# Kernel tuning notes

Measured on AMD Instinct MI355X. Metric: run time of the kernel, lower is better.

Reference implementation:

```python
import jax, jax.numpy as jnp
import numpy as np

N, L, D1, D2, K, C, T = 50000, 1024, 512, 256, 64, 2, 49


def setup_inputs() -> dict:
    key = jax.random.key(0)
    ks = jax.random.split(key, 20)
    s = 0.02
    return {
        "h": jax.random.normal(ks[0], (N, L), dtype=jnp.float32),
        "tabular": jax.random.normal(ks[1], (1, T), dtype=jnp.float32),
        "label": 1,
        # fc: Linear(1024,512)+ReLU
        "W_fc": jax.random.normal(ks[2], (L, D1)) * s, "b_fc": jnp.zeros((D1,)),
        # gated attention net
        "Wa": jax.random.normal(ks[3], (D1, D2)) * s, "ba": jnp.zeros((D2,)),
        "Wb": jax.random.normal(ks[4], (D1, D2)) * s, "bb": jnp.zeros((D2,)),
        "Wc": jax.random.normal(ks[5], (D2, 1)) * s, "bc": jnp.zeros((1,)),
        # per-class instance classifiers Linear(512,2), stacked [C, D1, 2]
        "W_inst": jax.random.normal(ks[6], (C, D1, 2)) * s, "b_inst": jnp.zeros((C, 2)),
        # MultiHeadAttention (1 head)
        "W_img": jax.random.normal(ks[7], (D1, 1)) * s, "b_img": jnp.zeros((1,)),
        "W_tab": jax.random.normal(ks[8], (T, T)) * s, "b_tab": jnp.zeros((T,)),
        # bag classifier Linear(512+49, 2)
        "W_cls": jax.random.normal(ks[9], (D1 + T, C)) * s, "b_cls": jnp.zeros((C,)),
    }


def _forward(h, tabular, label, W_fc, b_fc, Wa, ba, Wb, bb, Wc, bc,
             W_inst, b_inst, W_img, b_img, W_tab, b_tab, W_cls, b_cls):
    # attention_net: fc + ReLU then gated attention
    h512 = jax.nn.relu(h @ W_fc + b_fc)                       # [N, 512]
    a = jnp.tanh(h512 @ Wa + ba)                              # [N, 256]
    b = jax.nn.sigmoid(h512 @ Wb + bb)                        # [N, 256]
    A = ((a * b) @ Wc + bc).T                                 # [1, N]
    A_raw = A
    A = jax.nn.softmax(A, axis=1)                             # [1, N]

    # instance eval: top-k positive / top-k negative selection + tiny classifier + CE
    scores = A[0]                                             # [N]
    _, top_p_ids = jax.lax.top_k(scores, K)
    _, top_n_ids = jax.lax.top_k(-scores, K)
    all_inst = jnp.concatenate([h512[top_p_ids], h512[top_n_ids]], axis=0)  # [2K, 512]
    targets = jnp.concatenate([jnp.ones((K,), jnp.int32), jnp.zeros((K,), jnp.int32)])

    def inst_loss(Wi, bi):
        logits = all_inst @ Wi + bi                           # [2K, 2]
        logp = jax.nn.log_softmax(logits, axis=1)
        return -jnp.mean(logp[jnp.arange(2 * K), targets])

    losses = jax.vmap(inst_loss)(W_inst, b_inst)              # [C]
    onehot = jax.nn.one_hot(label, C, dtype=losses.dtype)
    total_inst_loss = jnp.sum(onehot * losses)                # only in-class classifier contributes

    # attention pooling
    M = A @ h512                                              # [1, 512]

    # MultiHeadAttention (1 head): gated image feature + softmax-gated tabular feature
    img_score = jax.nn.sigmoid(M @ W_img + b_img)             # [1, 1]
    tab_score = jax.nn.softmax(tabular @ W_tab + b_tab, axis=1)  # [1, 49]
    concat = jnp.concatenate([img_score * M, tab_score * tabular], axis=1)  # [1, 561]

    logits = concat @ W_cls + b_cls                           # [1, 2]
    Y_prob = jax.nn.softmax(logits, axis=1)
    Y_hat = jnp.argmax(logits, axis=1)
    return logits, Y_prob, Y_hat, A_raw, total_inst_loss


def reference(h, tabular, label, W_fc, b_fc, Wa, ba, Wb, bb, Wc, bc,
              W_inst, b_inst, W_img, b_img, W_tab, b_tab, W_cls, b_cls):
    return _forward(h, tabular, label, W_fc, b_fc, Wa, ba, Wb, bb, Wc, bc,
                    W_inst, b_inst, W_img, b_img, W_tab, b_tab, W_cls, b_cls)
```

## Files before the change

kernel.cpp:

```cpp
#include <hip/hip_runtime.h>
#include <stdint.h>

typedef __bf16 bf16x8 __attribute__((ext_vector_type(8)));
typedef float f32x4 __attribute__((ext_vector_type(4)));
typedef unsigned short u16;
typedef unsigned int u32;

#define N_INST 50000
#define NPAD   50048
#define LIN    1024
#define D1     512
#define D2     256
#define TOPK   64
#define TDIM   49
#define NBIN   65536
#define CAND_MAX 8192
#define ZERO_DW (520 + 128 + 16 + NBIN)

__device__ __forceinline__ float b2f(u16 u) {
    union { float f; u32 i; } x; x.i = ((u32)u) << 16; return x.f;
}
__device__ __forceinline__ u16 f2b(float f) {
    union { float f; u32 i; } x; x.f = f;
    u32 r = x.i + 0x7FFFu + ((x.i >> 16) & 1u);
    return (u16)(r >> 16);
}
__device__ __forceinline__ void gload16(const void* g, void* l) {
    __builtin_amdgcn_global_load_lds((const __attribute__((address_space(1))) void*)g,
                                     (__attribute__((address_space(3))) void*)l, 16, 0, 0);
}
__device__ __forceinline__ u32 swz(int row, int bytecol) {
    return (u32)(row * 128 + (bytecol ^ ((row & 7) << 4)));
}

__global__ void pack_w(const float* __restrict__ W_fc, const float* __restrict__ Wa,
                       const float* __restrict__ Wb, u16* __restrict__ WfcT,
                       u16* __restrict__ WaT, u16* __restrict__ WbT, u32* __restrict__ zbase) {
    int gt = blockIdx.x * blockDim.x + threadIdx.x;
    int nthr = gridDim.x * blockDim.x;
    for (int z = gt; z < ZERO_DW; z += nthr) zbase[z] = 0u;
    for (int e = gt; e < D1 * LIN; e += nthr) {
        int n = e >> 10, k = e & 1023;
        WfcT[e] = f2b(W_fc[(size_t)k * D1 + n]);
    }
    for (int f = gt; f < D2 * D1; f += nthr) {
        int j = f >> 9, k = f & 511;
        WaT[f] = f2b(Wa[(size_t)k * D2 + j]);
        WbT[f] = f2b(Wb[(size_t)k * D2 + j]);
    }
}

__global__ __launch_bounds__(512, 2)
void gemm_fc(const float* __restrict__ h, const u16* __restrict__ WfcT,
             const float* __restrict__ b_fc, u16* __restrict__ h512) {
    __shared__ __align__(16) u16 lA[128 * 64];
    __shared__ __align__(16) u16 lB[256 * 64];
    const int tid = threadIdx.x;
    const int lane = tid & 63, wid = tid >> 6;
    const int wr = wid >> 2, wc = wid & 3;
    const int lanelo = lane & 15, lanehi = lane >> 4;
    const int row0 = blockIdx.y * 128;
    const int col0 = blockIdx.x * 256;

    const int arow = tid >> 2;
    const int aseg = tid & 3;
    int srow = row0 + arow; if (srow >= N_INST) srow = N_INST - 1;
    const float* abase = h + (size_t)srow * LIN + aseg * 16;
    u16* aw0 = (u16*)((char*)lA + swz(arow, aseg * 32));
    u16* aw1 = (u16*)((char*)lA + swz(arow, aseg * 32 + 16));

    f32x4 acc[4][4];
    const f32x4 z4 = {0.f, 0.f, 0.f, 0.f};
    #pragma unroll
    for (int m = 0; m < 4; ++m)
        #pragma unroll
        for (int n = 0; n < 4; ++n) acc[m][n] = z4;

    float4 a0, a1, a2, a3;
    { const float4* ap = (const float4*)abase; a0 = ap[0]; a1 = ap[1]; a2 = ap[2]; a3 = ap[3]; }

    for (int kt = 0; kt < LIN / 64; ++kt) {
        #pragma unroll
        for (int q = 0; q < 4; ++q) {
            int c = tid + 512 * q;
            int col = c >> 3, d8 = c & 7;
            int k8 = d8 ^ (col & 7);
            gload16(WfcT + (size_t)(col0 + col) * LIN + kt * 64 + k8 * 8, (char*)lB + c * 16);
        }
        {
            bf16x8 w0, w1;
            w0[0] = (__bf16)a0.x; w0[1] = (__bf16)a0.y; w0[2] = (__bf16)a0.z; w0[3] = (__bf16)a0.w;
            w0[4] = (__bf16)a1.x; w0[5] = (__bf16)a1.y; w0[6] = (__bf16)a1.z; w0[7] = (__bf16)a1.w;
            w1[0] = (__bf16)a2.x; w1[1] = (__bf16)a2.y; w1[2] = (__bf16)a2.z; w1[3] = (__bf16)a2.w;
            w1[4] = (__bf16)a3.x; w1[5] = (__bf16)a3.y; w1[6] = (__bf16)a3.z; w1[7] = (__bf16)a3.w;
            *(bf16x8*)aw0 = w0;
            *(bf16x8*)aw1 = w1;
        }
        __syncthreads();
        if (kt + 1 < LIN / 64) {
            const float4* ap = (const float4*)(abase + (kt + 1) * 64);
            a0 = ap[0]; a1 = ap[1]; a2 = ap[2]; a3 = ap[3];
        }
        #pragma unroll
        for (int kk = 0; kk < 2; ++kk) {
            bf16x8 af[4], bfr[4];
            #pragma unroll
            for (int m = 0; m < 4; ++m) {
                int row = wr * 64 + m * 16 + lanelo;
                af[m] = *(const bf16x8*)((char*)lA + swz(row, kk * 64 + lanehi * 16));
            }
            #pragma unroll
            for (int n = 0; n < 4; ++n) {
                int col = wc * 64 + n * 16 + lanelo;
                bfr[n] = *(const bf16x8*)((char*)lB + swz(col, kk * 64 + lanehi * 16));
            }
            #pragma unroll
            for (int m = 0; m < 4; ++m)
                #pragma unroll
                for (int n = 0; n < 4; ++n)
                    acc[m][n] = __builtin_amdgcn_mfma_f32_16x16x32_bf16(af[m], bfr[n], acc[m][n], 0, 0, 0);
        }
        __syncthreads();
    }
    #pragma unroll
    for (int n = 0; n < 4; ++n) {
        int col = col0 + wc * 64 + n * 16 + lanelo;
        float bias = b_fc[col];
        #pragma unroll
        for (int m = 0; m < 4; ++m) {
            int rbase = row0 + wr * 64 + m * 16 + 4 * lanehi;
            #pragma unroll
            for (int r = 0; r < 4; ++r) {
                float v = acc[m][n][r] + bias;
                v = v > 0.f ? v : 0.f;
                h512[(size_t)(rbase + r) * D1 + col] = f2b(v);
            }
        }
    }
}

__global__ __launch_bounds__(512, 2)
void gemm_attn(const u16* __restrict__ h512, const u16* __restrict__ WaT,
               const u16* __restrict__ WbT, const float* __restrict__ ba,
               const float* __restrict__ bb, const float* __restrict__ Wc,
               const float* __restrict__ bc, float* __restrict__ araw,
               u32* __restrict__ uarr, u32* __restrict__ hist,
               float* __restrict__ Zacc, float* __restrict__ Mpart) {
    __shared__ __align__(16) u16 lA[128 * 64];
    __shared__ __align__(16) u16 lBa[256 * 64];
    __shared__ __align__(16) u16 lBb[256 * 64];
    __shared__ float rsum[128];
    __shared__ float sW[128];
    const int tid = threadIdx.x;
    const int lane = tid & 63, wid = tid >> 6;
    const int wr = wid >> 2, wc4 = wid & 3;
    const int lanelo = lane & 15, lanehi = lane >> 4;
    const int row0 = blockIdx.x * 128;

    f32x4 accA[4][4], accB[4][4];
    const f32x4 z4 = {0.f, 0.f, 0.f, 0.f};
    for (int m = 0; m < 4; ++m)
        for (int n = 0; n < 4; ++n) { accA[m][n] = z4; accB[m][n] = z4; }

    for (int kt = 0; kt < D1 / 64; ++kt) {
        #pragma unroll
        for (int q = 0; q < 2; ++q) {
            int c = tid + 512 * q;
            int row = c >> 3, d8 = c & 7;
            int k8 = d8 ^ (row & 7);
            gload16(h512 + (size_t)(row0 + row) * D1 + kt * 64 + k8 * 8, (char*)lA + c * 16);
        }
        #pragma unroll
        for (int q = 0; q < 4; ++q) {
            int c = tid + 512 * q;
            int col = c >> 3, d8 = c & 7;
            int k8 = d8 ^ (col & 7);
            gload16(WaT + (size_t)col * D1 + kt * 64 + k8 * 8, (char*)lBa + c * 16);
            gload16(WbT + (size_t)col * D1 + kt * 64 + k8 * 8, (char*)lBb + c * 16);
        }
        __syncthreads();
        #pragma unroll
        for (int kk = 0; kk < 2; ++kk) {
            bf16x8 af[4], ga[4], gb[4];
            #pragma unroll
            for (int m = 0; m < 4; ++m) {
                int row = wr * 64 + m * 16 + lanelo;
                af[m] = *(const bf16x8*)((char*)lA + swz(row, kk * 64 + lanehi * 16));
            }
            #pragma unroll
            for (int n = 0; n < 4; ++n) {
                int col = wc4 * 64 + n * 16 + lanelo;
                u32 off = swz(col, kk * 64 + lanehi * 16);
                ga[n] = *(const bf16x8*)((char*)lBa + off);
                gb[n] = *(const bf16x8*)((char*)lBb + off);
            }
            #pragma unroll
            for (int m = 0; m < 4; ++m)
                #pragma unroll
                for (int n = 0; n < 4; ++n) {
                    accA[m][n] = __builtin_amdgcn_mfma_f32_16x16x32_bf16(af[m], ga[n], accA[m][n], 0, 0, 0);
                    accB[m][n] = __builtin_amdgcn_mfma_f32_16x16x32_bf16(af[m], gb[n], accB[m][n], 0, 0, 0);
                }
        }
        __syncthreads();
    }

    if (tid < 128) rsum[tid] = 0.f;
    __syncthreads();

    float baR[4], bbR[4], wcR[4];
    #pragma unroll
    for (int n = 0; n < 4; ++n) {
        int j = wc4 * 64 + n * 16 + lanelo;
        baR[n] = ba[j]; bbR[n] = bb[j]; wcR[n] = Wc[j];
    }
    #pragma unroll
    for (int m = 0; m < 4; ++m) {
        #pragma unroll
        for (int r = 0; r < 4; ++r) {
            float s = 0.f;
            #pragma unroll
            for (int n = 0; n < 4; ++n) {
                float av = accA[m][n][r] + baR[n];
                float bv = accB[m][n][r] + bbR[n];
                float p = tanhf(av) / (1.f + expf(-bv));
                s += p * wcR[n];
            }
            s += __shfl_xor(s, 1); s += __shfl_xor(s, 2);
            s += __shfl_xor(s, 4); s += __shfl_xor(s, 8);
            if (lanelo == 0) atomicAdd(&rsum[wr * 64 + m * 16 + 4 * lanehi + r], s);
        }
    }
    __syncthreads();

    if (tid < 128) {
        int rg = row0 + tid;
        float e = 0.f;
        if (rg < N_INST) {
            float a = rsum[tid] + bc[0];
            araw[rg] = a;
            u32 bits = __float_as_uint(a);
            u32 key = (bits & 0x80000000u) ? ~bits : (bits | 0x80000000u);
            uarr[rg] = key;
            atomicAdd(&hist[key >> 16], 1u);
            e = expf(a);
        }
        sW[tid] = e;
    }
    __syncthreads();
    if (tid < 128) {
        float e = sW[tid];
        for (int o = 32; o > 0; o >>= 1) e += __shfl_xor(e, o);
        if (lane == 0) atomicAdd(Zacc, e);
    }
    float accM = 0.f;
    for (int i = 0; i < 128; ++i)
        accM += sW[i] * b2f(h512[(size_t)(row0 + i) * D1 + tid]);
    atomicAdd(&Mpart[tid], accM);
}

__global__ void topk_collect(const u32* __restrict__ hist, const u32* __restrict__ uarr,
                             int* __restrict__ ctl, int* __restrict__ ids,
                             u32* __restrict__ cV0, int* __restrict__ cI0,
                             u32* __restrict__ cV1, int* __restrict__ cI1) {
    __shared__ int part[256];
    __shared__ int sp0, sb0, sp1, sb1;
    const int t = threadIdx.x;
    const uint4* h4 = (const uint4*)hist;
    int s = 0;
    for (int j = 0; j < 64; ++j) {
        uint4 v = h4[t * 64 + j];
        s += (int)(v.x + v.y + v.z + v.w);
    }
    part[t] = s;
    __syncthreads();
    for (int off = 1; off < 256; off <<= 1) {
        int v = part[t];
        int a = (t >= off) ? part[t - off] : 0;
        __syncthreads();
        part[t] = v + a;
        __syncthreads();
    }
    int run = part[t] - s;
    for (int j = 0; j < 64; ++j) {
        uint4 v = h4[t * 64 + j];
        int c4[4]; c4[0] = (int)v.x; c4[1] = (int)v.y; c4[2] = (int)v.z; c4[3] = (int)v.w;
        #pragma unroll
        for (int e = 0; e < 4; ++e) {
            int cnt = c4[e];
            if (cnt > 0) {
                int b = t * 256 + j * 4 + e;
                int less = run, greater = N_INST - run - cnt;
                if (greater < TOPK && greater + cnt >= TOPK) { sp0 = b; sb0 = greater; }
                if (less < TOPK && less + cnt >= TOPK)       { sp1 = b; sb1 = less; }
            }
            run += cnt;
        }
    }
    __syncthreads();
    const int p0 = sp0, p1 = sp1;
    if (blockIdx.x == 0 && t == 0) { ctl[0] = sp0; ctl[1] = sb0; ctl[2] = sp1; ctl[3] = sb1; }

    int gt = blockIdx.x * blockDim.x + t;
    int nthr = gridDim.x * blockDim.x;
    for (int i = gt; i < N_INST; i += nthr) {
        u32 v = uarr[i];
        int b = (int)(v >> 16);
        if (b > p0)       { int p = atomicAdd(&ctl[8], 1);  ids[p] = i; }
        else if (b == p0) { int p = atomicAdd(&ctl[9], 1);  if (p < CAND_MAX) { cV0[p] = v; cI0[p] = i; } }
        if (b < p1)       { int p = atomicAdd(&ctl[10], 1); ids[TOPK + p] = i; }
        else if (b == p1) { int p = atomicAdd(&ctl[11], 1); if (p < CAND_MAX) { cV1[p] = v; cI1[p] = i; } }
    }
}

__global__ void tail_fused(const int* __restrict__ ctl,
                           const u32* __restrict__ cV0, const int* __restrict__ cI0,
                           const u32* __restrict__ cV1, const int* __restrict__ cI1,
                           int* __restrict__ ids, const u16* __restrict__ h512,
                           const float* __restrict__ W_inst, const float* __restrict__ b_inst,
                           const int* __restrict__ label, const float* __restrict__ Mpart,
                           const float* __restrict__ Zacc, const float* __restrict__ tabular,
                           const float* __restrict__ W_img, const float* __restrict__ b_img,
                           const float* __restrict__ W_tab, const float* __restrict__ b_tab,
                           const float* __restrict__ W_cls, const float* __restrict__ b_cls,
                           float* __restrict__ d_out) {
    __shared__ int h8[256];
    __shared__ int eq[2048];
    __shared__ int s_d1, s_k1, s_d2, s_fill, s_eqc;
    __shared__ float lsum;
    __shared__ float sM[512];
    __shared__ float stab[TDIM];
    __shared__ float red0[256], red1[256];
    __shared__ float simg;
    const int tid = threadIdx.x;
    const int lane = tid & 63, wid = tid >> 6;

    for (int mode = 0; mode < 2; ++mode) {
        int basem = ctl[mode * 2 + 1];
        int need = TOPK - basem;
        int ccnt = ctl[9 + mode * 2];
        if (ccnt > CAND_MAX) ccnt = CAND_MAX;
        const u32* cV = mode ? cV1 : cV0;
        const int* cI = mode ? cI1 : cI0;
        int* dst = ids + mode * TOPK;
        h8[tid] = 0; __syncthreads();
        for (int i = tid; i < ccnt; i += 256) atomicAdd(&h8[(cV[i] >> 8) & 255u], 1);
        __syncthreads();
        if (tid == 0) {
            int acc = 0, d, k = need;
            if (mode == 0) { for (d = 255; d >= 0; --d) { acc += h8[d]; if (acc >= k) break; } }
            else           { for (d = 0; d < 256; ++d)  { acc += h8[d]; if (acc >= k) break; } }
            s_d1 = d; s_k1 = k - (acc - h8[d]);
        }
        __syncthreads();
        int d1 = s_d1, k1 = s_k1;
        h8[tid] = 0; __syncthreads();
        for (int i = tid; i < ccnt; i += 256) {
            u32 v = cV[i];
            if (((v >> 8) & 255u) == (u32)d1) atomicAdd(&h8[v & 255u], 1);
        }
        __syncthreads();
        if (tid == 0) {
            int acc = 0, d, k = k1;
            if (mode == 0) { for (d = 255; d >= 0; --d) { acc += h8[d]; if (acc >= k) break; } }
            else           { for (d = 0; d < 256; ++d)  { acc += h8[d]; if (acc >= k) break; } }
            s_d2 = d; s_fill = 0; s_eqc = 0;
        }
        __syncthreads();
        u32 vth = ((u32)ctl[mode * 2] << 16) | ((u32)d1 << 8) | (u32)s_d2;
        for (int i = tid; i < ccnt; i += 256) {
            u32 v = cV[i];
            bool better = mode == 0 ? (v > vth) : (v < vth);
            if (better)        { int p = atomicAdd(&s_fill, 1); dst[basem + p] = cI[i]; }
            else if (v == vth) { int p = atomicAdd(&s_eqc, 1);  if (p < 2048) eq[p] = cI[i]; }
        }
        __syncthreads();
        if (tid == 0) {
            int have = basem + s_fill;
            int rem = TOPK - have;
            int m = s_eqc < 2048 ? s_eqc : 2048;
            int last = -1;
            for (int q = 0; q < rem; ++q) {
                int best = 0x7FFFFFFF;
                for (int s = 0; s < m; ++s) { int ix = eq[s]; if (ix > last && ix < best) best = ix; }
                dst[have + q] = best; last = best;
            }
        }
        __syncthreads();
    }

    if (tid == 0) lsum = 0.f;
    __syncthreads();
    const int lab = label[0];
    const float* W = W_inst + (size_t)lab * (D1 * 2);
    const float b0 = b_inst[lab * 2 + 0], b1 = b_inst[lab * 2 + 1];
    for (int i = 0; i < 32; ++i) {
        int r = wid * 32 + i;
        int row = ids[r];
        float s0 = 0.f, s1 = 0.f;
        for (int s = 0; s < 8; ++s) {
            int j = lane + 64 * s;
            float hv = b2f(h512[(size_t)row * D1 + j]);
            s0 += hv * W[j * 2 + 0];
            s1 += hv * W[j * 2 + 1];
        }
        for (int o = 32; o > 0; o >>= 1) { s0 += __shfl_xor(s0, o); s1 += __shfl_xor(s1, o); }
        if (lane == 0) {
            float l0 = s0 + b0, l1 = s1 + b1;
            float mx = fmaxf(l0, l1);
            float lse = mx + logf(expf(l0 - mx) + expf(l1 - mx));
            float lt = (r < TOPK) ? l1 : l0;
            atomicAdd(&lsum, lse - lt);
        }
    }
    __syncthreads();
    if (tid == 0) d_out[50005] = lsum / 128.f;

    float invZ = 1.f / Zacc[0];
    sM[tid] = Mpart[tid] * invZ;
    sM[tid + 256] = Mpart[tid + 256] * invZ;
    red0[tid] = sM[tid] * W_img[tid] + sM[tid + 256] * W_img[tid + 256];
    __syncthreads();
    for (int o = 128; o > 0; o >>= 1) { if (tid < o) red0[tid] += red0[tid + o]; __syncthreads(); }
    if (tid == 0) simg = 1.f / (1.f + expf(-(red0[0] + b_img[0])));
    if (tid < TDIM) {
        float t = b_tab[tid];
        for (int kx = 0; kx < TDIM; ++kx) t += tabular[kx] * W_tab[kx * TDIM + tid];
        stab[tid] = t;
    }
    __syncthreads();
    if (tid == 0) {
        float mx = stab[0];
        for (int o = 1; o < TDIM; ++o) mx = fmaxf(mx, stab[o]);
        float ss = 0.f;
        for (int o = 0; o < TDIM; ++o) { float e = expf(stab[o] - mx); stab[o] = e; ss += e; }
        for (int o = 0; o < TDIM; ++o) stab[o] = (stab[o] / ss) * tabular[o];
    }
    __syncthreads();
    float img = simg;
    float a0 = 0.f, a1 = 0.f;
    for (int j = tid; j < D1 + TDIM; j += 256) {
        float w = (j < D1) ? img * sM[j] : stab[j - D1];
        a0 += w * W_cls[j * 2 + 0];
        a1 += w * W_cls[j * 2 + 1];
    }
    red0[tid] = a0; red1[tid] = a1;
    __syncthreads();
    for (int o = 128; o > 0; o >>= 1) {
        if (tid < o) { red0[tid] += red0[tid + o]; red1[tid] += red1[tid + o]; }
        __syncthreads();
    }
    if (tid == 0) {
        float l0 = red0[0] + b_cls[0];
        float l1 = red1[0] + b_cls[1];
        d_out[0] = l0; d_out[1] = l1;
        float mx = fmaxf(l0, l1);
        float e0 = expf(l0 - mx), e1 = expf(l1 - mx);
        d_out[2] = e0 / (e0 + e1);
        d_out[3] = e1 / (e0 + e1);
        d_out[4] = (l1 > l0) ? 1.f : 0.f;
    }
}

extern "C" void kernel_launch(void* const* d_in, const int* in_sizes, int n_in,
                              void* d_out, int out_size, void* d_ws, size_t ws_size,
                              hipStream_t stream) {
    const float* h       = (const float*)d_in[0];
    const float* tabular = (const float*)d_in[1];
    const int*   label   = (const int*)d_in[2];
    const float* W_fc    = (const float*)d_in[3];
    const float* b_fc    = (const float*)d_in[4];
    const float* Wa      = (const float*)d_in[5];
    const float* ba      = (const float*)d_in[6];
    const float* Wb      = (const float*)d_in[7];
    const float* bb      = (const float*)d_in[8];
    const float* Wc      = (const float*)d_in[9];
    const float* bc      = (const float*)d_in[10];
    const float* W_inst  = (const float*)d_in[11];
    const float* b_inst  = (const float*)d_in[12];
    const float* W_img   = (const float*)d_in[13];
    const float* b_img   = (const float*)d_in[14];
    const float* W_tab   = (const float*)d_in[15];
    const float* b_tab   = (const float*)d_in[16];
    const float* W_cls   = (const float*)d_in[17];
    const float* b_cls   = (const float*)d_in[18];
    float* out = (float*)d_out;

    u16* h512 = (u16*)d_ws;
    u16* WfcT = h512 + (size_t)NPAD * D1;
    u16* WaT  = WfcT + (size_t)D1 * LIN;
    u16* WbT  = WaT + (size_t)D2 * D1;
    u32* uarr = (u32*)(WbT + (size_t)D2 * D1);
    float* accum = (float*)(uarr + NPAD);
    float* Zacc  = accum;
    float* Mpart = accum + 8;
    int* ids = (int*)(accum + 8 + D1);
    int* ctl = ids + 128;
    u32* hist = (u32*)(ctl + 16);
    u32* cV0 = hist + NBIN;
    int* cI0 = (int*)(cV0 + CAND_MAX);
    u32* cV1 = (u32*)(cI0 + CAND_MAX);
    int* cI1 = (int*)(cV1 + CAND_MAX);

    pack_w<<<dim3(256), dim3(256), 0, stream>>>(W_fc, Wa, Wb, WfcT, WaT, WbT, (u32*)accum);
    gemm_fc<<<dim3(2, NPAD / 128), dim3(512), 0, stream>>>(h, WfcT, b_fc, h512);
    gemm_attn<<<dim3(NPAD / 128), dim3(512), 0, stream>>>(
        h512, WaT, WbT, ba, bb, Wc, bc, out + 5, uarr, hist, Zacc, Mpart);
    topk_collect<<<dim3(128), dim3(256), 0, stream>>>(hist, uarr, ctl, ids, cV0, cI0, cV1, cI1);
    tail_fused<<<dim3(1), dim3(256), 0, stream>>>(
        ctl, cV0, cI0, cV1, cI1, ids, h512, W_inst, b_inst, label,
        Mpart, Zacc, tabular, W_img, b_img, W_tab, b_tab, W_cls, b_cls, out);
}
```

Baseline: 308.7 us.

## Load fc A operand straight to registers and double-buffer B tiles in LDS

The fc GEMM no longer stages the fp32 activations through LDS. Each wave loads its A rows directly from global memory in the MFMA fragment layout, converts them to bf16 in registers and prefetches the next k-tile. The weight tile B is double-buffered in shared memory, so each iteration needs one barrier instead of two. The trade-off is that the four waves sharing a row group each fetch the same A rows, which multiplies global/L2 traffic for the largest input. The larger prefetch register set also risks spills or lower occupancy.

```diff
diff --git a/kernel.cpp b/kernel.cpp
--- a/kernel.cpp
+++ b/kernel.cpp
@@ -53,8 +53,7 @@
 __global__ __launch_bounds__(512, 2)
 void gemm_fc(const float* __restrict__ h, const u16* __restrict__ WfcT,
              const float* __restrict__ b_fc, u16* __restrict__ h512) {
-    __shared__ __align__(16) u16 lA[128 * 64];
-    __shared__ __align__(16) u16 lB[256 * 64];
+    __shared__ __align__(16) u16 lB[2][256 * 64];
     const int tid = threadIdx.x;
     const int lane = tid & 63, wid = tid >> 6;
     const int wr = wid >> 2, wc = wid & 3;
@@ -62,12 +61,20 @@
     const int row0 = blockIdx.y * 128;
     const int col0 = blockIdx.x * 256;
 
-    const int arow = tid >> 2;
-    const int aseg = tid & 3;
-    int srow = row0 + arow; if (srow >= N_INST) srow = N_INST - 1;
-    const float* abase = h + (size_t)srow * LIN + aseg * 16;
-    u16* aw0 = (u16*)((char*)lA + swz(arow, aseg * 32));
-    u16* aw1 = (u16*)((char*)lA + swz(arow, aseg * 32 + 16));
+    const float* arow0;
+    const float* arow1;
+    const float* arow2;
+    const float* arow3;
+    {
+        int r0 = row0 + wr * 64 + 0 * 16 + lanelo; if (r0 >= N_INST) r0 = N_INST - 1;
+        int r1 = row0 + wr * 64 + 1 * 16 + lanelo; if (r1 >= N_INST) r1 = N_INST - 1;
+        int r2 = row0 + wr * 64 + 2 * 16 + lanelo; if (r2 >= N_INST) r2 = N_INST - 1;
+        int r3 = row0 + wr * 64 + 3 * 16 + lanelo; if (r3 >= N_INST) r3 = N_INST - 1;
+        arow0 = h + (size_t)r0 * LIN + lanehi * 8;
+        arow1 = h + (size_t)r1 * LIN + lanehi * 8;
+        arow2 = h + (size_t)r2 * LIN + lanehi * 8;
+        arow3 = h + (size_t)r3 * LIN + lanehi * 8;
+    }
 
     f32x4 acc[4][4];
     const f32x4 z4 = {0.f, 0.f, 0.f, 0.f};
@@ -76,52 +83,69 @@
         #pragma unroll
         for (int n = 0; n < 4; ++n) acc[m][n] = z4;
 
-    float4 a0, a1, a2, a3;
-    { const float4* ap = (const float4*)abase; a0 = ap[0]; a1 = ap[1]; a2 = ap[2]; a3 = ap[3]; }
+    float4 apre[4][2][2];
+    #define LOAD_A(kt_)                                                              \
+        do {                                                                         \
+            const float* rs_[4] = {arow0, arow1, arow2, arow3};                      \
+            _Pragma("unroll")                                                        \
+            for (int m_ = 0; m_ < 4; ++m_) {                                         \
+                _Pragma("unroll")                                                    \
+                for (int kk_ = 0; kk_ < 2; ++kk_) {                                  \
+                    apre[m_][kk_][0] = *(const float4*)(rs_[m_] + (kt_) * 64 + kk_ * 32);     \
+                    apre[m_][kk_][1] = *(const float4*)(rs_[m_] + (kt_) * 64 + kk_ * 32 + 4); \
+                }                                                                    \
+            }                                                                        \
+        } while (0)
+
+    #define STAGE_B(buf_, kt_)                                                       \
+        do {                                                                         \
+            _Pragma("unroll")                                                        \
+            for (int q_ = 0; q_ < 4; ++q_) {                                         \
+                int c_ = tid + 512 * q_;                                             \
+                int col_ = c_ >> 3, d8_ = c_ & 7;                                    \
+                int k8_ = d8_ ^ (col_ & 7);                                          \
+                gload16(WfcT + (size_t)(col0 + col_) * LIN + (kt_) * 64 + k8_ * 8,   \
+                        (char*)lB[buf_] + c_ * 16);                                  \
+            }                                                                        \
+        } while (0)
+
+    LOAD_A(0);
+    STAGE_B(0, 0);
 
     for (int kt = 0; kt < LIN / 64; ++kt) {
-        #pragma unroll
-        for (int q = 0; q < 4; ++q) {
-            int c = tid + 512 * q;
-            int col = c >> 3, d8 = c & 7;
-            int k8 = d8 ^ (col & 7);
-            gload16(WfcT + (size_t)(col0 + col) * LIN + kt * 64 + k8 * 8, (char*)lB + c * 16);
-        }
-        {
-            bf16x8 w0, w1;
-            w0[0] = (__bf16)a0.x; w0[1] = (__bf16)a0.y; w0[2] = (__bf16)a0.z; w0[3] = (__bf16)a0.w;
-            w0[4] = (__bf16)a1.x; w0[5] = (__bf16)a1.y; w0[6] = (__bf16)a1.z; w0[7] = (__bf16)a1.w;
-            w1[0] = (__bf16)a2.x; w1[1] = (__bf16)a2.y; w1[2] = (__bf16)a2.z; w1[3] = (__bf16)a2.w;
-            w1[4] = (__bf16)a3.x; w1[5] = (__bf16)a3.y; w1[6] = (__bf16)a3.z; w1[7] = (__bf16)a3.w;
-            *(bf16x8*)aw0 = w0;
-            *(bf16x8*)aw1 = w1;
-        }
-        __syncthreads();
-        if (kt + 1 < LIN / 64) {
-            const float4* ap = (const float4*)(abase + (kt + 1) * 64);
-            a0 = ap[0]; a1 = ap[1]; a2 = ap[2]; a3 = ap[3];
-        }
+        const int cur = kt & 1;
+        __syncthreads();
+        if (kt + 1 < LIN / 64) STAGE_B(cur ^ 1, kt + 1);
+        bf16x8 abf[4][2];
+        #pragma unroll
+        for (int m = 0; m < 4; ++m)
+            #pragma unroll
+            for (int kk = 0; kk < 2; ++kk) {
+                float4 x = apre[m][kk][0], y = apre[m][kk][1];
+                bf16x8 w;
+                w[0] = (__bf16)x.x; w[1] = (__bf16)x.y; w[2] = (__bf16)x.z; w[3] = (__bf16)x.w;
+                w[4] = (__bf16)y.x; w[5] = (__bf16)y.y; w[6] = (__bf16)y.z; w[7] = (__bf16)y.w;
+                abf[m][kk] = w;
+            }
+        if (kt + 1 < LIN / 64) LOAD_A(kt + 1);
         #pragma unroll
         for (int kk = 0; kk < 2; ++kk) {
-            bf16x8 af[4], bfr[4];
-            #pragma unroll
-            for (int m = 0; m < 4; ++m) {
-                int row = wr * 64 + m * 16 + lanelo;
-                af[m] = *(const bf16x8*)((char*)lA + swz(row, kk * 64 + lanehi * 16));
-            }
+            bf16x8 bfr[4];
             #pragma unroll
             for (int n = 0; n < 4; ++n) {
                 int col = wc * 64 + n * 16 + lanelo;
-                bfr[n] = *(const bf16x8*)((char*)lB + swz(col, kk * 64 + lanehi * 16));
+                bfr[n] = *(const bf16x8*)((char*)lB[cur] + swz(col, kk * 64 + lanehi * 16));
             }
             #pragma unroll
             for (int m = 0; m < 4; ++m)
                 #pragma unroll
                 for (int n = 0; n < 4; ++n)
-                    acc[m][n] = __builtin_amdgcn_mfma_f32_16x16x32_bf16(af[m], bfr[n], acc[m][n], 0, 0, 0);
-        }
-        __syncthreads();
-    }
+                    acc[m][n] = __builtin_amdgcn_mfma_f32_16x16x32_bf16(abf[m][kk], bfr[n], acc[m][n], 0, 0, 0);
+        }
+    }
+    #undef LOAD_A
+    #undef STAGE_B
+
     #pragma unroll
     for (int n = 0; n < 4; ++n) {
         int col = col0 + wc * 64 + n * 16 + lanelo;
```

New measurement: 457.5 us. 48.2% more time.

## Pre-convert h to bf16 and use a bf16-input 128x128 FC GEMM

Applied to the files above, without the earlier changes.

A combined pack kernel now also converts the full fp32 `h` matrix to a padded bf16 copy in workspace. A new FC GEMM then streams bf16 A tiles into LDS via global_load_lds, with 128x128 tiles and 256 threads. The goal is to drop the in-loop fp32-to-bf16 conversion and halve the A bytes each tile reads. The cost is an extra full write and read of a large bf16 intermediate, more column blocks that each re-read A, and an unswizzled LDS layout that may cause bank conflicts. The new path only runs when the workspace is large enough; otherwise the old fp32 kernel is kept as a fallback.

```diff
diff --git a/kernel.cpp b/kernel.cpp
--- a/kernel.cpp
+++ b/kernel.cpp
@@ -33,12 +33,32 @@
     return (u32)(row * 128 + (bytecol ^ ((row & 7) << 4)));
 }
 
-__global__ void pack_w(const float* __restrict__ W_fc, const float* __restrict__ Wa,
-                       const float* __restrict__ Wb, u16* __restrict__ WfcT,
-                       u16* __restrict__ WaT, u16* __restrict__ WbT, u32* __restrict__ zbase) {
+__global__ void pack_all(const float* __restrict__ h, const float* __restrict__ W_fc,
+                         const float* __restrict__ Wa, const float* __restrict__ Wb,
+                         u16* __restrict__ hb, u16* __restrict__ WfcT,
+                         u16* __restrict__ WaT, u16* __restrict__ WbT,
+                         u32* __restrict__ zbase) {
     int gt = blockIdx.x * blockDim.x + threadIdx.x;
     int nthr = gridDim.x * blockDim.x;
     for (int z = gt; z < ZERO_DW; z += nthr) zbase[z] = 0u;
+    if (hb) {
+        const int HC = NPAD * LIN / 8;
+        for (int c = gt; c < HC; c += nthr) {
+            int row = c >> 7;
+            uint4 o;
+            if (row < N_INST) {
+                const float4* p = (const float4*)(h + (size_t)c * 8);
+                float4 v0 = p[0], v1 = p[1];
+                o.x = (u32)f2b(v0.x) | ((u32)f2b(v0.y) << 16);
+                o.y = (u32)f2b(v0.z) | ((u32)f2b(v0.w) << 16);
+                o.z = (u32)f2b(v1.x) | ((u32)f2b(v1.y) << 16);
+                o.w = (u32)f2b(v1.z) | ((u32)f2b(v1.w) << 16);
+            } else {
+                o.x = o.y = o.z = o.w = 0u;
+            }
+            *(uint4*)(hb + (size_t)c * 8) = o;
+        }
+    }
     for (int e = gt; e < D1 * LIN; e += nthr) {
         int n = e >> 10, k = e & 1023;
         WfcT[e] = f2b(W_fc[(size_t)k * D1 + n]);
@@ -50,9 +70,74 @@
     }
 }
 
+__global__ __launch_bounds__(256, 3)
+void gemm_fc_bf(const u16* __restrict__ hb, const u16* __restrict__ WfcT,
+                const float* __restrict__ b_fc, u16* __restrict__ h512) {
+    __shared__ __align__(16) u16 lA[128 * 64];
+    __shared__ __align__(16) u16 lB[128 * 64];
+    const int tid = threadIdx.x;
+    const int lane = tid & 63, wid = tid >> 6;
+    const int wr = wid >> 1, wc = wid & 1;
+    const int lanelo = lane & 15, lanehi = lane >> 4;
+    const int row0 = blockIdx.y * 128;
+    const int col0 = blockIdx.x * 128;
+
+    f32x4 acc[4][4];
+    const f32x4 z4 = {0.f, 0.f, 0.f, 0.f};
+    for (int m = 0; m < 4; ++m)
+        for (int n = 0; n < 4; ++n) acc[m][n] = z4;
+
+    for (int kt = 0; kt < LIN / 64; ++kt) {
+        #pragma unroll
+        for (int q = 0; q < 4; ++q) {
+            int c = tid + 256 * q;
+            int row = c >> 3, k8 = c & 7;
+            gload16(hb + (size_t)(row0 + row) * LIN + kt * 64 + k8 * 8, (char*)lA + c * 16);
+        }
+        #pragma unroll
+        for (int q = 0; q < 4; ++q) {
+            int c = tid + 256 * q;
+            int col = c >> 3, k8 = c & 7;
+            gload16(WfcT + (size_t)(col0 + col) * LIN + kt * 64 + k8 * 8, (char*)lB + c * 16);
+        }
+        __syncthreads();
+        #pragma unroll
+        for (int kk = 0; kk < 2; ++kk) {
+            bf16x8 af[4], bfr[4];
+            #pragma unroll
+            for (int m = 0; m < 4; ++m)
+                af[m] = *(const bf16x8*)((char*)lA + (wr * 64 + m * 16 + lanelo) * 128 + kk * 64 + lanehi * 16);
+            #pragma unroll
+            for (int n = 0; n < 4; ++n)
+                bfr[n] = *(const bf16x8*)((char*)lB + (wc * 64 + n * 16 + lanelo) * 128 + kk * 64 + lanehi * 16);
+            #pragma unroll
+            for (int m = 0; m < 4; ++m)
+                #pragma unroll
+                for (int n = 0; n < 4; ++n)
+                    acc[m][n] = __builtin_amdgcn_mfma_f32_16x16x32_bf16(af[m], bfr[n], acc[m][n], 0, 0, 0);
+        }
+        __syncthreads();
+    }
+    #pragma unroll
+    for (int n = 0; n < 4; ++n) {
+        int col = col0 + wc * 64 + n * 16 + lanelo;
+        float bias = b_fc[col];
+        #pragma unroll
+        for (int m = 0; m < 4; ++m) {
+            int rbase = row0 + wr * 64 + m * 16 + 4 * lanehi;
+            #pragma unroll
+            for (int r = 0; r < 4; ++r) {
+                float v = acc[m][n][r] + bias;
+                v = v > 0.f ? v : 0.f;
+                h512[(size_t)(rbase + r) * D1 + col] = f2b(v);
+            }
+        }
+    }
+}
+
 __global__ __launch_bounds__(512, 2)
-void gemm_fc(const float* __restrict__ h, const u16* __restrict__ WfcT,
-             const float* __restrict__ b_fc, u16* __restrict__ h512) {
+void gemm_fc_f32(const float* __restrict__ h, const u16* __restrict__ WfcT,
+                 const float* __restrict__ b_fc, u16* __restrict__ h512) {
     __shared__ __align__(16) u16 lA[128 * 64];
     __shared__ __align__(16) u16 lB[256 * 64];
     const int tid = threadIdx.x;
@@ -71,9 +156,7 @@
 
     f32x4 acc[4][4];
     const f32x4 z4 = {0.f, 0.f, 0.f, 0.f};
-    #pragma unroll
     for (int m = 0; m < 4; ++m)
-        #pragma unroll
         for (int n = 0; n < 4; ++n) acc[m][n] = z4;
 
     float4 a0, a1, a2, a3;
@@ -501,9 +584,18 @@
     int* cI0 = (int*)(cV0 + CAND_MAX);
     u32* cV1 = (u32*)(cI0 + CAND_MAX);
     int* cI1 = (int*)(cV1 + CAND_MAX);
-
-    pack_w<<<dim3(256), dim3(256), 0, stream>>>(W_fc, Wa, Wb, WfcT, WaT, WbT, (u32*)accum);
-    gemm_fc<<<dim3(2, NPAD / 128), dim3(512), 0, stream>>>(h, WfcT, b_fc, h512);
+    u16* hb  = (u16*)(cI1 + CAND_MAX);
+    size_t need = ((char*)(hb + (size_t)NPAD * LIN)) - (char*)d_ws;
+    bool fast = ws_size >= need;
+
+    pack_all<<<dim3(2048), dim3(256), 0, stream>>>(h, W_fc, Wa, Wb,
+                                                   fast ? hb : (u16*)nullptr, WfcT, WaT, WbT,
+                                                   (u32*)accum);
+    if (fast) {
+        gemm_fc_bf<<<dim3(4, NPAD / 128), dim3(256), 0, stream>>>(hb, WfcT, b_fc, h512);
+    } else {
+        gemm_fc_f32<<<dim3(2, NPAD / 128), dim3(512), 0, stream>>>(h, WfcT, b_fc, h512);
+    }
     gemm_attn<<<dim3(NPAD / 128), dim3(512), 0, stream>>>(
         h512, WaT, WbT, ba, bb, Wc, bc, out + 5, uarr, hist, Zacc, Mpart);
     topk_collect<<<dim3(128), dim3(256), 0, stream>>>(hist, uarr, ctl, ids, cV0, cI0, cV1, cI1);
```

Measured after the change: 324.6 us. +5.2%, slower.

## Double-buffer LDS tiles in fc GEMM to overlap staging with MFMA

Applied to the files above, without the earlier changes.

The fc GEMM's A and B shared-memory tiles become two buffers. The next k-tile is staged into the idle buffer while MFMAs run on the current one, which drops the trailing barrier so each k-iteration has one __syncthreads instead of two. The cost is that LDS per block doubles to about 96KB. That likely no longer allows two 512-thread blocks per CU, as the launch bounds request, so occupancy may fall and hide less latency.

```diff
diff --git a/kernel.cpp b/kernel.cpp
--- a/kernel.cpp
+++ b/kernel.cpp
@@ -53,8 +53,8 @@
 __global__ __launch_bounds__(512, 2)
 void gemm_fc(const float* __restrict__ h, const u16* __restrict__ WfcT,
              const float* __restrict__ b_fc, u16* __restrict__ h512) {
-    __shared__ __align__(16) u16 lA[128 * 64];
-    __shared__ __align__(16) u16 lB[256 * 64];
+    __shared__ __align__(16) u16 lA[2][128 * 64];
+    __shared__ __align__(16) u16 lB[2][256 * 64];
     const int tid = threadIdx.x;
     const int lane = tid & 63, wid = tid >> 6;
     const int wr = wid >> 2, wc = wid & 3;
@@ -66,8 +66,8 @@
     const int aseg = tid & 3;
     int srow = row0 + arow; if (srow >= N_INST) srow = N_INST - 1;
     const float* abase = h + (size_t)srow * LIN + aseg * 16;
-    u16* aw0 = (u16*)((char*)lA + swz(arow, aseg * 32));
-    u16* aw1 = (u16*)((char*)lA + swz(arow, aseg * 32 + 16));
+    const u32 awo0 = swz(arow, aseg * 32);
+    const u32 awo1 = swz(arow, aseg * 32 + 16);
 
     f32x4 acc[4][4];
     const f32x4 z4 = {0.f, 0.f, 0.f, 0.f};
@@ -77,29 +77,42 @@
         for (int n = 0; n < 4; ++n) acc[m][n] = z4;
 
     float4 a0, a1, a2, a3;
-    { const float4* ap = (const float4*)abase; a0 = ap[0]; a1 = ap[1]; a2 = ap[2]; a3 = ap[3]; }
+
+    #define LOAD_A(kt_)                                                     \
+        do {                                                                \
+            const float4* ap_ = (const float4*)(abase + (kt_) * 64);        \
+            a0 = ap_[0]; a1 = ap_[1]; a2 = ap_[2]; a3 = ap_[3];             \
+        } while (0)
+
+    #define STAGE(buf_, kt_)                                                             \
+        do {                                                                             \
+            _Pragma("unroll")                                                            \
+            for (int q_ = 0; q_ < 4; ++q_) {                                             \
+                int c_ = tid + 512 * q_;                                                 \
+                int col_ = c_ >> 3, d8_ = c_ & 7;                                        \
+                int k8_ = d8_ ^ (col_ & 7);                                              \
+                gload16(WfcT + (size_t)(col0 + col_) * LIN + (kt_) * 64 + k8_ * 8,       \
+                        (char*)lB[buf_] + c_ * 16);                                      \
+            }                                                                            \
+            bf16x8 w0_, w1_;                                                             \
+            w0_[0] = (__bf16)a0.x; w0_[1] = (__bf16)a0.y; w0_[2] = (__bf16)a0.z; w0_[3] = (__bf16)a0.w; \
+            w0_[4] = (__bf16)a1.x; w0_[5] = (__bf16)a1.y; w0_[6] = (__bf16)a1.z; w0_[7] = (__bf16)a1.w; \
+            w1_[0] = (__bf16)a2.x; w1_[1] = (__bf16)a2.y; w1_[2] = (__bf16)a2.z; w1_[3] = (__bf16)a2.w; \
+            w1_[4] = (__bf16)a3.x; w1_[5] = (__bf16)a3.y; w1_[6] = (__bf16)a3.z; w1_[7] = (__bf16)a3.w; \
+            *(bf16x8*)((char*)lA[buf_] + awo0) = w0_;                                    \
+            *(bf16x8*)((char*)lA[buf_] + awo1) = w1_;                                    \
+        } while (0)
+
+    LOAD_A(0);
+    STAGE(0, 0);
+    LOAD_A(1);
 
     for (int kt = 0; kt < LIN / 64; ++kt) {
-        #pragma unroll
-        for (int q = 0; q < 4; ++q) {
-            int c = tid + 512 * q;
-            int col = c >> 3, d8 = c & 7;
-            int k8 = d8 ^ (col & 7);
-            gload16(WfcT + (size_t)(col0 + col) * LIN + kt * 64 + k8 * 8, (char*)lB + c * 16);
-        }
-        {
-            bf16x8 w0, w1;
-            w0[0] = (__bf16)a0.x; w0[1] = (__bf16)a0.y; w0[2] = (__bf16)a0.z; w0[3] = (__bf16)a0.w;
-            w0[4] = (__bf16)a1.x; w0[5] = (__bf16)a1.y; w0[6] = (__bf16)a1.z; w0[7] = (__bf16)a1.w;
-            w1[0] = (__bf16)a2.x; w1[1] = (__bf16)a2.y; w1[2] = (__bf16)a2.z; w1[3] = (__bf16)a2.w;
-            w1[4] = (__bf16)a3.x; w1[5] = (__bf16)a3.y; w1[6] = (__bf16)a3.z; w1[7] = (__bf16)a3.w;
-            *(bf16x8*)aw0 = w0;
-            *(bf16x8*)aw1 = w1;
-        }
+        const int cur = kt & 1;
         __syncthreads();
         if (kt + 1 < LIN / 64) {
-            const float4* ap = (const float4*)(abase + (kt + 1) * 64);
-            a0 = ap[0]; a1 = ap[1]; a2 = ap[2]; a3 = ap[3];
+            STAGE(cur ^ 1, kt + 1);
+            if (kt + 2 < LIN / 64) LOAD_A(kt + 2);
         }
         #pragma unroll
         for (int kk = 0; kk < 2; ++kk) {
@@ -107,12 +120,12 @@
             #pragma unroll
             for (int m = 0; m < 4; ++m) {
                 int row = wr * 64 + m * 16 + lanelo;
-                af[m] = *(const bf16x8*)((char*)lA + swz(row, kk * 64 + lanehi * 16));
+                af[m] = *(const bf16x8*)((char*)lA[cur] + swz(row, kk * 64 + lanehi * 16));
             }
             #pragma unroll
             for (int n = 0; n < 4; ++n) {
                 int col = wc * 64 + n * 16 + lanelo;
-                bfr[n] = *(const bf16x8*)((char*)lB + swz(col, kk * 64 + lanehi * 16));
+                bfr[n] = *(const bf16x8*)((char*)lB[cur] + swz(col, kk * 64 + lanehi * 16));
             }
             #pragma unroll
             for (int m = 0; m < 4; ++m)
@@ -120,8 +133,10 @@
                 for (int n = 0; n < 4; ++n)
                     acc[m][n] = __builtin_amdgcn_mfma_f32_16x16x32_bf16(af[m], bfr[n], acc[m][n], 0, 0, 0);
         }
-        __syncthreads();
-    }
+    }
+    #undef LOAD_A
+    #undef STAGE
+
     #pragma unroll
     for (int n = 0; n < 4; ++n) {
         int col = col0 + wc * 64 + n * 16 + lanelo;
```

New measurement: 312.3 us. Within noise of the previous version (+1.2%).
